# Kernel optimization log

Measured on AMD Instinct MI355X. Metric: run time of the kernel, lower is better.

The kernel has to match this reference:

```python
import jax, jax.numpy as jnp
import numpy as np

MAX_FRAMES = 1000

def _sigmoid_factors(factor, shift, n=MAX_FRAMES):
    x = np.arange(n, dtype=np.float32)
    a = np.clip(x * factor - shift, -80.0, 80.0)
    return jnp.asarray(1.9 / (1.0 + np.exp(a)) + 0.4, dtype=jnp.float32)

F_FACTORS = _sigmoid_factors(1.0, 1.0)  # f_factor=1.0, f_discount=1.0

def setup_inputs() -> dict:
    key = jax.random.key(0)
    k1, _ = jax.random.split(key)
    B, T, D = 32, 1000, 512
    data = jax.random.normal(k1, (B, T, D), dtype=jnp.float32)
    threshold = jnp.full((1,), 30.0, dtype=jnp.float32)  # agent.linear_threshold
    return {"data": data, "threshold": threshold}

def _forward_single(data, thr):
    # data: [T, D]. avg_rep=False, overlapping=False path of forward_single.
    T, D = data.shape
    pref = jnp.cumsum(data, axis=0)  # pref[i-1] = sum(data[:i])
    idx = jnp.arange(1, T)

    def step(carry, xs):
        rep, f_i, ind, start_sum = carry  # rep=data[ind], start_sum=sum(data[:ind])
        i, frame, csum_i = xs             # csum_i = sum(data[:i])
        dist = jnp.linalg.norm(rep - frame)
        boundary = dist > thr * F_FACTORS[jnp.minimum(f_i, MAX_FRAMES - 1)]
        seg_len = (i - ind).astype(data.dtype)
        mean = (csum_i - start_sum) / seg_len  # data[ind:i].mean(0)
        new_rep = jnp.where(boundary, frame, rep)
        new_f = jnp.where(boundary, 0, f_i + 1)
        new_ind = jnp.where(boundary, i, ind)
        new_start = jnp.where(boundary, csum_i, start_sum)
        out_mean = jnp.where(boundary, mean, jnp.zeros_like(mean))
        return (new_rep, new_f, new_ind, new_start), (boundary, out_mean)

    init = (data[0], jnp.int32(0), jnp.int32(0), jnp.zeros((D,), data.dtype))
    _, (flags, means) = jax.lax.scan(step, init, (idx, data[1:], pref[:-1]))
    # Fixed-shape padded result: means[t] is valid iff flags[t] (torch version
    # stacks only the valid rows; final `and False` tail-append is dead code).
    return means, flags

def reference(data, threshold):
    thr = threshold[0]
    means, flags = jax.vmap(_forward_single, in_axes=(0, None))(data, thr)
    return means, flags  # [B, T-1, D] padded segment means, [B, T-1] validity mask
```

## Files before the change

kernel.cpp:

```cpp
#include <hip/hip_runtime.h>
#include <math.h>


typedef float v4 __attribute__((ext_vector_type(4)));

#define T_F    1000
#define D_DIM  512
#define NV4    128
#define BAND_W 4
#define RUNB   16
#define RPBB   63

__device__ __forceinline__ float wave_sum64(float x) {
  x += __shfl_xor(x, 1);
  x += __shfl_xor(x, 2);
  x += __shfl_xor(x, 4);
  x += __shfl_xor(x, 8);
  x += __shfl_xor(x, 16);
  x += __shfl_xor(x, 32);
  return x;
}

__device__ __forceinline__ v4 sel4(bool c, v4 a, v4 b) {
  v4 r;
  r.x = c ? a.x : b.x; r.y = c ? a.y : b.y;
  r.z = c ? a.z : b.z; r.w = c ? a.w : b.w;
  return r;
}

__device__ __forceinline__ unsigned pack8(unsigned x, unsigned y) {
  unsigned a = x & 0x0F0F0F0Fu; a |= a >> 4;
  unsigned p = (a & 0xFFu) | ((a >> 8) & 0xFF00u);
  unsigned b = y & 0x0F0F0F0Fu; b |= b >> 4;
  unsigned q = (b & 0xFFu) | ((b >> 8) & 0xFF00u);
  return p | (q << 16);
}

__global__ __launch_bounds__(256)
void band_kernel(const float* __restrict__ data, const float* __restrict__ thrp,
                 unsigned char* __restrict__ deltab, int B) {
  const int lane = threadIdx.x & 63;
  const int wid  = threadIdx.x >> 6;
  const int run  = blockIdx.x * 4 + wid;
  if (run >= B * RPBB) return;
  const int b   = run / RPBB;
  const int s0i = (run % RPBB) * RUNB;

  const v4* __restrict__ dp = reinterpret_cast<const v4*>(data) + (size_t)b * T_F * NV4;
  unsigned char* __restrict__ dbp = deltab + (size_t)b * 1024;

  const int   wl  = lane & 3;
  const float thr = thrp[0];
  float Ff  = 1.9f / (1.0f + expf((float)wl - 1.0f)) + 0.4f;
  float tt  = thr * Ff;
  const float tf2l = tt * tt;

  const int q0 = lane, q1 = 64 + lane;
  v4 ra[8], rb[8];
#pragma unroll
  for (int d = 0; d < 8; ++d) {
    int t = s0i + d; if (t > T_F - 1) t = T_F - 1;
    ra[d] = dp[(size_t)t * NV4 + q0];
    rb[d] = dp[(size_t)t * NV4 + q1];
  }

#pragma unroll
  for (int u = 0; u < RUNB; ++u) {
    const int s  = s0i + u;
    const int su = u & 7;
    float p[BAND_W];
#pragma unroll
    for (int w = 0; w < BAND_W; ++w) {
      const int sj = (u + 1 + w) & 7;
      v4 d0 = ra[su] - ra[sj];
      v4 d1 = rb[su] - rb[sj];
      p[w] = d0.x*d0.x + d0.y*d0.y + d0.z*d0.z + d0.w*d0.w
           + d1.x*d1.x + d1.y*d1.y + d1.z*d1.z + d1.w*d1.w;
    }
    int tn = s + 8; if (tn > T_F - 1) tn = T_F - 1;
    v4 na = dp[(size_t)tn * NV4 + q0];
    v4 nb = dp[(size_t)tn * NV4 + q1];

#pragma unroll
    for (int w = 0; w < BAND_W; ++w) {
      p[w] += __shfl_xor(p[w], 1);
      p[w] += __shfl_xor(p[w], 2);
      p[w] += __shfl_xor(p[w], 4);
    }
    const bool bt0 = (lane & 1) != 0, bt1 = (lane & 2) != 0;
    float q0v  = bt0 ? p[1] : p[0];
    float q1v  = bt0 ? p[3] : p[2];
    float comb = bt1 ? q1v : q0v;
    comb += __shfl_xor(comb, 8);
    comb += __shfl_xor(comb, 16);
    comb += __shfl_xor(comb, 32);
    bool valid = (s + 1 + wl) <= (T_F - 1);
    bool bnd   = valid && (comb > tf2l);
    unsigned long long m = __ballot(bnd);
    int delta = __ffsll((unsigned long long)(m & 0xFull));
    if (lane == 0 && s <= T_F - 2) dbp[s] = (unsigned char)delta;

    ra[su] = na; rb[su] = nb;
  }
}

__global__ __launch_bounds__(64, 1)
void scan_kernel(const float* __restrict__ data, const float* __restrict__ thrp,
                 const unsigned char* __restrict__ deltab,
                 int* __restrict__ scan_out, int B) {
  const int b    = blockIdx.x;
  const int lane = threadIdx.x;
  const v4* __restrict__ dp = reinterpret_cast<const v4*>(data) + (size_t)b * T_F * NV4;
  int* __restrict__ so = scan_out + (size_t)b * 1024;

#pragma unroll
  for (int j = 0; j < 16; ++j) so[j * 64 + lane] = -1;

  const uint4 dd = reinterpret_cast<const uint4*>(deltab + (size_t)b * 1024)[lane];
  unsigned plo = pack8(dd.x, dd.y);
  unsigned phi = pack8(dd.z, dd.w);

  __builtin_amdgcn_s_waitcnt(0);

  int s = 0;
  bool need_exact = false;
  while (s < T_F - 1) {
    unsigned lo = (unsigned)__builtin_amdgcn_readlane((int)plo, s >> 4);
    unsigned hi = (unsigned)__builtin_amdgcn_readlane((int)phi, s >> 4);
    unsigned word = (s & 8) ? hi : lo;
    int delta = (word >> ((s & 7) * 4)) & 15;
    if (delta == 0) { need_exact = (s < T_F - 1 - BAND_W); break; }
    s += delta;
    if (lane == 0) so[s] = s - delta;
  }

  if (need_exact) {
    const float thr = thrp[0];
    const int q0 = lane, q1 = 64 + lane;
    int ind = s, f = 0;
    v4 rep0 = dp[(size_t)ind * NV4 + q0];
    v4 rep1 = dp[(size_t)ind * NV4 + q1];
    for (int i = s + 1; i <= T_F - 1; ++i) {
      float av = fminf((float)f - 1.0f, 80.0f);
      float Ff = 1.9f / (1.0f + expf(av)) + 0.4f;
      float t2 = thr * Ff; t2 *= t2;
      v4 x0 = dp[(size_t)i * NV4 + q0];
      v4 x1 = dp[(size_t)i * NV4 + q1];
      v4 d0 = rep0 - x0, d1 = rep1 - x1;
      float part = d0.x*d0.x + d0.y*d0.y + d0.z*d0.z + d0.w*d0.w
                 + d1.x*d1.x + d1.y*d1.y + d1.z*d1.z + d1.w*d1.w;
      float d2 = wave_sum64(part);
      bool bnd = d2 > t2;
      if (bnd) {
        if (lane == 0) so[i] = ind;
        ind = i; f = 0; rep0 = x0; rep1 = x1;
      } else {
        f += 1;
      }
    }
  }
}

__global__ __launch_bounds__(256)
void mean_kernel(const float* __restrict__ data, const int* __restrict__ scan_out,
                 float* __restrict__ out, int B) {
  const int lane = threadIdx.x & 63;
  const int wv   = threadIdx.x >> 6;
  const int b    = blockIdx.y;
  const int i0   = blockIdx.x * 16 + wv * 4;

  const v4* __restrict__ dp  = reinterpret_cast<const v4*>(data) + (size_t)b * T_F * NV4;
  const int* __restrict__ so = scan_out + (size_t)b * 1024;
  v4* __restrict__ mp        = reinterpret_cast<v4*>(out) + (size_t)b * (T_F - 1) * NV4;
  float* __restrict__ fl     = out + (size_t)B * (T_F - 1) * D_DIM + (size_t)b * (T_F - 1);
  const int q0 = lane, q1 = 64 + lane;

  const int4 sv = *reinterpret_cast<const int4*>(so + i0);
  const int sarr[4] = {sv.x, sv.y, sv.z, sv.w};

  const v4 z = {0.f, 0.f, 0.f, 0.f};
#pragma unroll
  for (int q = 0; q < 4; ++q) {
    const int i = i0 + q;
    if (i < 1 || i > T_F - 1) continue;
    const int s = sarr[q];
    if (s < 0) {
      __builtin_nontemporal_store(z, &mp[(size_t)(i - 1) * NV4 + q0]);
      __builtin_nontemporal_store(z, &mp[(size_t)(i - 1) * NV4 + q1]);
      if (lane == 0) __builtin_nontemporal_store(0.0f, &fl[i - 1]);
      continue;
    }
    const int len = i - s;
    v4 a0 = z, a1 = z;
    if (len <= BAND_W) {
#pragma unroll
      for (int j = 0; j < BAND_W; ++j) {
        const int t = (j < len) ? (s + j) : (i - 1);
        const float msk = (j < len) ? 1.0f : 0.0f;
        v4 x0 = dp[(size_t)t * NV4 + q0];
        v4 x1 = dp[(size_t)t * NV4 + q1];
        a0.x += x0.x * msk; a0.y += x0.y * msk; a0.z += x0.z * msk; a0.w += x0.w * msk;
        a1.x += x1.x * msk; a1.y += x1.y * msk; a1.z += x1.z * msk; a1.w += x1.w * msk;
      }
    } else {
      for (int t = s; t < i; ++t) {
        a0 += dp[(size_t)t * NV4 + q0];
        a1 += dp[(size_t)t * NV4 + q1];
      }
    }
    const float inv = 1.0f / (float)len;
    a0.x *= inv; a0.y *= inv; a0.z *= inv; a0.w *= inv;
    a1.x *= inv; a1.y *= inv; a1.z *= inv; a1.w *= inv;
    __builtin_nontemporal_store(a0, &mp[(size_t)(i - 1) * NV4 + q0]);
    __builtin_nontemporal_store(a1, &mp[(size_t)(i - 1) * NV4 + q1]);
    if (lane == 0) __builtin_nontemporal_store(1.0f, &fl[i - 1]);
  }
}

__global__ __launch_bounds__(64, 1)
void dist_agg_mono(const float* __restrict__ data,
                   const float* __restrict__ thrp,
                   float* __restrict__ out, int B) {
  const int b    = blockIdx.x;
  const int lane = threadIdx.x;
  const float thr = thrp[0];
  const v4* __restrict__ dp = reinterpret_cast<const v4*>(data) + (size_t)b * T_F * NV4;
  v4* __restrict__ mp       = reinterpret_cast<v4*>(out) + (size_t)b * (T_F - 1) * NV4;
  float* __restrict__ fp    = out + (size_t)B * (T_F - 1) * D_DIM + (size_t)b * (T_F - 1);
  const int s0 = lane, s1 = 64 + lane;

  v4 rep0 = dp[s0], rep1 = dp[s1];
  v4 cs0  = rep0,  cs1  = rep1;
  v4 ss0  = {0.f,0.f,0.f,0.f}, ss1 = {0.f,0.f,0.f,0.f};
  int ind = 0, fi = 0;
  const float F0     = 1.9f / (1.0f + expf(-1.0f)) + 0.4f;
  const float tf0    = thr * F0;
  const float tf2_f0 = tf0 * tf0;
  float tf2 = tf2_f0;

  for (int i = 1; i < T_F; ++i) {
    float an      = fminf((float)fi, 80.0f);
    float Fn      = 1.9f / (1.0f + expf(an)) + 0.4f;
    float tn      = thr * Fn;
    float tf2_inc = tn * tn;
    v4 fa = dp[(size_t)i * NV4 + s0];
    v4 fb = dp[(size_t)i * NV4 + s1];
    v4 d0 = rep0 - fa, d1 = rep1 - fb;
    float part = d0.x*d0.x + d0.y*d0.y + d0.z*d0.z + d0.w*d0.w
               + d1.x*d1.x + d1.y*d1.y + d1.z*d1.z + d1.w*d1.w;
    float dist2 = wave_sum64(part);
    bool bnd = dist2 > tf2;
    float inv = 1.0f / (float)(i - ind);
    v4 df0 = cs0 - ss0, df1 = cs1 - ss1;
    v4 m0, m1, z = {0.f,0.f,0.f,0.f};
    m0.x = df0.x*inv; m0.y = df0.y*inv; m0.z = df0.z*inv; m0.w = df0.w*inv;
    m1.x = df1.x*inv; m1.y = df1.y*inv; m1.z = df1.z*inv; m1.w = df1.w*inv;
    mp[(size_t)(i-1) * NV4 + s0] = sel4(bnd, m0, z);
    mp[(size_t)(i-1) * NV4 + s1] = sel4(bnd, m1, z);
    if (lane == 0) fp[i-1] = bnd ? 1.0f : 0.0f;
    rep0 = sel4(bnd, fa, rep0); rep1 = sel4(bnd, fb, rep1);
    ss0  = sel4(bnd, cs0, ss0); ss1  = sel4(bnd, cs1, ss1);
    ind  = bnd ? i : ind;
    fi   = bnd ? 0 : fi + 1;
    tf2  = bnd ? tf2_f0 : tf2_inc;
    cs0 += fa; cs1 += fb;
  }
}

extern "C" void kernel_launch(void* const* d_in, const int* in_sizes, int n_in,
                              void* d_out, int out_size, void* d_ws, size_t ws_size,
                              hipStream_t stream) {
  const float* data = (const float*)d_in[0];
  const float* thr  = (const float*)d_in[1];
  float* out        = (float*)d_out;
  const int B = in_sizes[0] / (T_F * D_DIM);

  const size_t need = (size_t)B * 1024 + (size_t)B * 1024 * 4;

  if (ws_size >= need) {
    unsigned char* deltab = (unsigned char*)d_ws;
    int* scan_out = (int*)((unsigned char*)d_ws + (size_t)B * 1024);
    const int runs = B * RPBB;
    band_kernel<<<(runs + 3) / 4, 256, 0, stream>>>(data, thr, deltab, B);
    scan_kernel<<<B, 64, 0, stream>>>(data, thr, deltab, scan_out, B);
    mean_kernel<<<dim3(63, B), 256, 0, stream>>>(data, scan_out, out, B);
  } else {
    dist_agg_mono<<<B, 64, 0, stream>>>(data, thr, out, B);
  }
}
```

Before: 153.5 us.

## Fuse band, scan and mean kernels into one cooperative kernel with grid syncs

Replaces the three separate launches (band detection, sequential scan, segment mean) with one persistent cooperative kernel of 256 blocks × 512 threads. The phases are separated by grid-wide syncs and use grid-stride loops over waves. The goal is to remove inter-kernel launch gaps and tail drain between stages. In exchange it pays for two grid barriers, and the scan phase uses only 32 of 2048 waves while the rest sit idle at the barrier. The old three-kernel path stays as a fallback if the cooperative launch fails.

Result: slower. 210.8 us (+37.3%).

```diff
diff --git a/kernel.cpp b/kernel.cpp
--- a/kernel.cpp
+++ b/kernel.cpp
@@ -1,6 +1,9 @@
 #include <hip/hip_runtime.h>
+#include <hip/hip_cooperative_groups.h>
 #include <math.h>
 
+
+namespace cg = cooperative_groups;
 
 typedef float v4 __attribute__((ext_vector_type(4)));
 
@@ -10,6 +13,9 @@
 #define BAND_W 4
 #define RUNB   16
 #define RPBB   63
+#define CBLK   256
+#define CTHR   512
+#define CWAVES (CBLK * (CTHR / 64))
 
 __device__ __forceinline__ float wave_sum64(float x) {
   x += __shfl_xor(x, 1);
@@ -36,25 +42,9 @@
   return p | (q << 16);
 }
 
-__global__ __launch_bounds__(256)
-void band_kernel(const float* __restrict__ data, const float* __restrict__ thrp,
-                 unsigned char* __restrict__ deltab, int B) {
-  const int lane = threadIdx.x & 63;
-  const int wid  = threadIdx.x >> 6;
-  const int run  = blockIdx.x * 4 + wid;
-  if (run >= B * RPBB) return;
-  const int b   = run / RPBB;
-  const int s0i = (run % RPBB) * RUNB;
-
-  const v4* __restrict__ dp = reinterpret_cast<const v4*>(data) + (size_t)b * T_F * NV4;
-  unsigned char* __restrict__ dbp = deltab + (size_t)b * 1024;
-
-  const int   wl  = lane & 3;
-  const float thr = thrp[0];
-  float Ff  = 1.9f / (1.0f + expf((float)wl - 1.0f)) + 0.4f;
-  float tt  = thr * Ff;
-  const float tf2l = tt * tt;
-
+__device__ __forceinline__ void band_run(const v4* __restrict__ dp,
+                                         unsigned char* __restrict__ dbp,
+                                         int s0i, int lane, float tf2l, int wl) {
   const int q0 = lane, q1 = 64 + lane;
   v4 ra[8], rb[8];
 #pragma unroll
@@ -63,7 +53,6 @@
     ra[d] = dp[(size_t)t * NV4 + q0];
     rb[d] = dp[(size_t)t * NV4 + q1];
   }
-
 #pragma unroll
   for (int u = 0; u < RUNB; ++u) {
     const int s  = s0i + u;
@@ -80,7 +69,6 @@
     int tn = s + 8; if (tn > T_F - 1) tn = T_F - 1;
     v4 na = dp[(size_t)tn * NV4 + q0];
     v4 nb = dp[(size_t)tn * NV4 + q1];
-
 #pragma unroll
     for (int w = 0; w < BAND_W; ++w) {
       p[w] += __shfl_xor(p[w], 1);
@@ -99,28 +87,17 @@
     unsigned long long m = __ballot(bnd);
     int delta = __ffsll((unsigned long long)(m & 0xFull));
     if (lane == 0 && s <= T_F - 2) dbp[s] = (unsigned char)delta;
-
     ra[su] = na; rb[su] = nb;
   }
 }
 
-__global__ __launch_bounds__(64, 1)
-void scan_kernel(const float* __restrict__ data, const float* __restrict__ thrp,
-                 const unsigned char* __restrict__ deltab,
-                 int* __restrict__ scan_out, int B) {
-  const int b    = blockIdx.x;
-  const int lane = threadIdx.x;
-  const v4* __restrict__ dp = reinterpret_cast<const v4*>(data) + (size_t)b * T_F * NV4;
-  int* __restrict__ so = scan_out + (size_t)b * 1024;
-
-#pragma unroll
-  for (int j = 0; j < 16; ++j) so[j * 64 + lane] = -1;
-
-  const uint4 dd = reinterpret_cast<const uint4*>(deltab + (size_t)b * 1024)[lane];
+__device__ __forceinline__ void scan_batch(const v4* __restrict__ dp,
+                                           const float* __restrict__ thrp,
+                                           const unsigned char* __restrict__ dbp,
+                                           int* __restrict__ so, int lane) {
+  const uint4 dd = reinterpret_cast<const uint4*>(dbp)[lane];
   unsigned plo = pack8(dd.x, dd.y);
   unsigned phi = pack8(dd.z, dd.w);
-
-  __builtin_amdgcn_s_waitcnt(0);
 
   int s = 0;
   bool need_exact = false;
@@ -150,8 +127,7 @@
       float part = d0.x*d0.x + d0.y*d0.y + d0.z*d0.z + d0.w*d0.w
                  + d1.x*d1.x + d1.y*d1.y + d1.z*d1.z + d1.w*d1.w;
       float d2 = wave_sum64(part);
-      bool bnd = d2 > t2;
-      if (bnd) {
+      if (d2 > t2) {
         if (lane == 0) so[i] = ind;
         ind = i; f = 0; rep0 = x0; rep1 = x1;
       } else {
@@ -161,23 +137,14 @@
   }
 }
 
-__global__ __launch_bounds__(256)
-void mean_kernel(const float* __restrict__ data, const int* __restrict__ scan_out,
-                 float* __restrict__ out, int B) {
-  const int lane = threadIdx.x & 63;
-  const int wv   = threadIdx.x >> 6;
-  const int b    = blockIdx.y;
-  const int i0   = blockIdx.x * 16 + wv * 4;
-
-  const v4* __restrict__ dp  = reinterpret_cast<const v4*>(data) + (size_t)b * T_F * NV4;
-  const int* __restrict__ so = scan_out + (size_t)b * 1024;
-  v4* __restrict__ mp        = reinterpret_cast<v4*>(out) + (size_t)b * (T_F - 1) * NV4;
-  float* __restrict__ fl     = out + (size_t)B * (T_F - 1) * D_DIM + (size_t)b * (T_F - 1);
+__device__ __forceinline__ void mean_group(const v4* __restrict__ dp,
+                                           const int* __restrict__ so,
+                                           v4* __restrict__ mp,
+                                           float* __restrict__ fl,
+                                           int i0, int lane) {
   const int q0 = lane, q1 = 64 + lane;
-
   const int4 sv = *reinterpret_cast<const int4*>(so + i0);
   const int sarr[4] = {sv.x, sv.y, sv.z, sv.w};
-
   const v4 z = {0.f, 0.f, 0.f, 0.f};
 #pragma unroll
   for (int q = 0; q < 4; ++q) {
@@ -215,6 +182,91 @@
     __builtin_nontemporal_store(a1, &mp[(size_t)(i - 1) * NV4 + q1]);
     if (lane == 0) __builtin_nontemporal_store(1.0f, &fl[i - 1]);
   }
+}
+
+__global__ __launch_bounds__(CTHR)
+void fused_kernel(const float* __restrict__ data, const float* __restrict__ thrp,
+                  float* __restrict__ out, unsigned char* __restrict__ deltab,
+                  int* __restrict__ so_base, int B) {
+  const int lane = threadIdx.x & 63;
+  const int gw   = blockIdx.x * (CTHR / 64) + (threadIdx.x >> 6);
+  const float thr = thrp[0];
+
+  {
+    const int   wl  = lane & 3;
+    float Ff  = 1.9f / (1.0f + expf((float)wl - 1.0f)) + 0.4f;
+    float tt  = thr * Ff;
+    const float tf2l = tt * tt;
+    for (int r = gw; r < B * RPBB; r += CWAVES) {
+      const int b   = r / RPBB;
+      const int s0i = (r % RPBB) * RUNB;
+      band_run(reinterpret_cast<const v4*>(data) + (size_t)b * T_F * NV4,
+               deltab + (size_t)b * 1024, s0i, lane, tf2l, wl);
+    }
+    const int gt = blockIdx.x * CTHR + threadIdx.x;
+    for (int e = gt; e < B * 1024; e += CBLK * CTHR) so_base[e] = -1;
+  }
+  cg::this_grid().sync();
+
+  for (int b = gw; b < B; b += CWAVES) {
+    scan_batch(reinterpret_cast<const v4*>(data) + (size_t)b * T_F * NV4, thrp,
+               deltab + (size_t)b * 1024, so_base + (size_t)b * 1024, lane);
+  }
+  cg::this_grid().sync();
+
+  const int gpb = 250;
+  for (int g = gw; g < B * gpb; g += CWAVES) {
+    const int b  = g / gpb;
+    const int i0 = (g % gpb) * 4;
+    mean_group(reinterpret_cast<const v4*>(data) + (size_t)b * T_F * NV4,
+               so_base + (size_t)b * 1024,
+               reinterpret_cast<v4*>(out) + (size_t)b * (T_F - 1) * NV4,
+               out + (size_t)B * (T_F - 1) * D_DIM + (size_t)b * (T_F - 1),
+               i0, lane);
+  }
+}
+
+__global__ __launch_bounds__(256)
+void band_kernel(const float* __restrict__ data, const float* __restrict__ thrp,
+                 unsigned char* __restrict__ deltab, int B) {
+  const int lane = threadIdx.x & 63;
+  const int run  = blockIdx.x * 4 + (threadIdx.x >> 6);
+  if (run >= B * RPBB) return;
+  const int b   = run / RPBB;
+  const int s0i = (run % RPBB) * RUNB;
+  const int wl  = lane & 3;
+  const float thr = thrp[0];
+  float Ff  = 1.9f / (1.0f + expf((float)wl - 1.0f)) + 0.4f;
+  float tt  = thr * Ff;
+  band_run(reinterpret_cast<const v4*>(data) + (size_t)b * T_F * NV4,
+           deltab + (size_t)b * 1024, s0i, lane, tt * tt, wl);
+}
+
+__global__ __launch_bounds__(64, 1)
+void scan_kernel(const float* __restrict__ data, const float* __restrict__ thrp,
+                 const unsigned char* __restrict__ deltab,
+                 int* __restrict__ scan_out, int B) {
+  const int b    = blockIdx.x;
+  const int lane = threadIdx.x;
+  int* so = scan_out + (size_t)b * 1024;
+#pragma unroll
+  for (int j = 0; j < 16; ++j) so[j * 64 + lane] = -1;
+  __builtin_amdgcn_s_waitcnt(0);
+  scan_batch(reinterpret_cast<const v4*>(data) + (size_t)b * T_F * NV4, thrp,
+             deltab + (size_t)b * 1024, so, lane);
+}
+
+__global__ __launch_bounds__(256)
+void mean_kernel(const float* __restrict__ data, const int* __restrict__ scan_out,
+                 float* __restrict__ out, int B) {
+  const int lane = threadIdx.x & 63;
+  const int b    = blockIdx.y;
+  const int i0   = blockIdx.x * 16 + (threadIdx.x >> 6) * 4;
+  mean_group(reinterpret_cast<const v4*>(data) + (size_t)b * T_F * NV4,
+             scan_out + (size_t)b * 1024,
+             reinterpret_cast<v4*>(out) + (size_t)b * (T_F - 1) * NV4,
+             out + (size_t)B * (T_F - 1) * D_DIM + (size_t)b * (T_F - 1),
+             i0, lane);
 }
 
 __global__ __launch_bounds__(64, 1)
@@ -280,10 +332,20 @@
   if (ws_size >= need) {
     unsigned char* deltab = (unsigned char*)d_ws;
     int* scan_out = (int*)((unsigned char*)d_ws + (size_t)B * 1024);
-    const int runs = B * RPBB;
-    band_kernel<<<(runs + 3) / 4, 256, 0, stream>>>(data, thr, deltab, B);
-    scan_kernel<<<B, 64, 0, stream>>>(data, thr, deltab, scan_out, B);
-    mean_kernel<<<dim3(63, B), 256, 0, stream>>>(data, scan_out, out, B);
+
+    void* args[6];
+    const float* a0 = data; const float* a1 = thr; float* a2 = out;
+    unsigned char* a3 = deltab; int* a4 = scan_out; int a5 = B;
+    args[0] = &a0; args[1] = &a1; args[2] = &a2;
+    args[3] = &a3; args[4] = &a4; args[5] = &a5;
+    hipError_t err = hipLaunchCooperativeKernel(
+        (void*)fused_kernel, dim3(CBLK), dim3(CTHR), args, 0, stream);
+    if (err != hipSuccess) {
+      const int runs = B * RPBB;
+      band_kernel<<<(runs + 3) / 4, 256, 0, stream>>>(data, thr, deltab, B);
+      scan_kernel<<<B, 64, 0, stream>>>(data, thr, deltab, scan_out, B);
+      mean_kernel<<<dim3(63, B), 256, 0, stream>>>(data, scan_out, out, B);
+    }
   } else {
     dist_agg_mono<<<B, 64, 0, stream>>>(data, thr, out, B);
   }
```
